# Performance work log

Measured on AMD Instinct MI355X. Metric: run time of the kernel, lower is better.

The kernel has to match this reference:

```python
import jax, jax.numpy as jnp
import numpy as np
from jax import lax

NH = 1024
CATS = 1024
B = 64
T = 512


def setup_inputs() -> dict:
    key = jax.random.key(0)
    ks = jax.random.split(key, 12)
    s_in = 1.0 / np.sqrt(CATS)
    s_h = 1.0 / np.sqrt(NH)
    return {
        "x": jax.random.normal(ks[0], (B, T, CATS), jnp.float32),
        "h0": jax.random.normal(ks[1], (B, NH), jnp.float32),
        # torch Linear weights are [out, in]
        "Wh": jax.random.uniform(ks[2], (NH, CATS), jnp.float32, -s_in, s_in),
        "Wz": jax.random.uniform(ks[3], (NH, CATS), jnp.float32, -s_in, s_in),
        "Wr": jax.random.uniform(ks[4], (NH, CATS), jnp.float32, -s_in, s_in),
        "Uh": jax.random.uniform(ks[5], (NH, NH), jnp.float32, -s_h, s_h),
        "Uz": jax.random.uniform(ks[6], (NH, NH), jnp.float32, -s_h, s_h),
        "Ur": jax.random.uniform(ks[7], (NH, NH), jnp.float32, -s_h, s_h),
        "bz": jax.random.uniform(ks[8], (NH,), jnp.float32, -s_h, s_h),
        "br": jax.random.uniform(ks[9], (NH,), jnp.float32, -s_h, s_h),
        "Wout": jax.random.uniform(ks[10], (CATS, NH), jnp.float32, -s_h, s_h),
    }


def _gru_last_h(x, h0, Wh, Wz, Wr, Uh, Uz, Ur, bz, br):
    # Precompute input projections as big GEMMs: [B,T,nh] each
    xh = jnp.einsum('btc,hc->bth', x, Wh)
    xz = jnp.einsum('btc,hc->bth', x, Wz)
    # Note: reset gate r is computed in the original but NEVER used in htilde
    # (htilde = tanh(Wh x + Uh h)); it does not affect the output, so we omit it.
    # Scan over time: inputs as [T, B, nh]
    seq = (jnp.swapaxes(xh, 0, 1), jnp.swapaxes(xz, 0, 1))

    def step(h, inp):
        xh_t, xz_t = inp
        z = jax.nn.sigmoid(xz_t + h @ Uz.T + bz)
        htilde = jnp.tanh(xh_t + h @ Uh.T)
        h_new = (1.0 - z) * h + z * htilde
        return h_new, None

    hT, _ = lax.scan(step, h0, seq)
    return hT  # [B, nh]


def reference(x, h0, Wh, Wz, Wr, Uh, Uz, Ur, bz, br, Wout):
    hT = _gru_last_h(x, h0, Wh, Wz, Wr, Uh, Uz, Ur, bz, br)
    return hT @ Wout.T  # [B, cats]
```

## Files before the change

kernel.cpp:

```cpp
#include <hip/hip_runtime.h>

typedef __attribute__((ext_vector_type(8))) short short8v;
typedef __attribute__((ext_vector_type(4))) short short4v;
typedef __attribute__((ext_vector_type(4))) float f32x4;
typedef __attribute__((ext_vector_type(4))) float float4v;
typedef unsigned long long u64;

#define NHID 1024
#define NCAT 1024
#define NB   64
#define NT   512

__device__ __forceinline__ short f2bf(float f) {
  union { float f; unsigned u; } c; c.f = f;
  unsigned r = (c.u + 0x7fffu + ((c.u >> 16) & 1u)) >> 16;
  return (short)r;
}

union HF { u64 q[2]; short8v v; };

__device__ __forceinline__ u64 ald(const u64* p) {
  return __hip_atomic_load(p, __ATOMIC_RELAXED, __HIP_MEMORY_SCOPE_AGENT);
}
__device__ __forceinline__ void ast(u64* p, u64 v) {
  __hip_atomic_store(p, v, __ATOMIC_RELAXED, __HIP_MEMORY_SCOPE_AGENT);
}

__global__ void cast_kernel(const float* __restrict__ x, const float* __restrict__ h0,
                            short* __restrict__ xb, short* __restrict__ hb0) {
  const long NX4 = (long)NB * NT * NCAT / 4;
  const long NH4 = (long)NB * NHID / 4;
  long i = (long)blockIdx.x * blockDim.x + threadIdx.x;
  long stride = (long)gridDim.x * blockDim.x;
  for (long j = i; j < NX4 + NH4; j += stride) {
    if (j < NH4) {
      float4v v = ((const float4v*)h0)[j];
      short4v s; s[0]=f2bf(v[0]); s[1]=f2bf(v[1]); s[2]=f2bf(v[2]); s[3]=f2bf(v[3]);
      ((short4v*)hb0)[j] = s;
    } else {
      long jj = j - NH4;
      float4v v = ((const float4v*)x)[jj];
      short4v s; s[0]=f2bf(v[0]); s[1]=f2bf(v[1]); s[2]=f2bf(v[2]); s[3]=f2bf(v[3]);
      ((short4v*)xb)[jj] = s;
    }
  }
}

__global__ __launch_bounds__(256, 1) void gru_kernel(
    const float* __restrict__ h0, const float* __restrict__ Wh, const float* __restrict__ Wz,
    const float* __restrict__ Uh, const float* __restrict__ Uz, const float* __restrict__ bz,
    const float* __restrict__ Wout, const short* __restrict__ xb,
    short* __restrict__ hbuf0, short* __restrict__ hbuf1,
    unsigned* __restrict__ flags, float* __restrict__ out)
{
  extern __shared__ char smem[];
  short8v* ufr = (short8v*)smem;
  float*   red = (float*)(smem + 131072);
  short*   rp  = (short*)(smem + 131072 + 12288);

  const int tid  = threadIdx.x;
  const int lane = tid & 63;
  const int wv   = tid >> 6;
  const int mt   = blockIdx.x >> 6;
  const int cg   = blockIdx.x & 63;
  const int col  = lane & 15;
  const int quad = lane >> 4;
  const int kq   = quad * 8;
  const int jg   = cg * 16 + col;

  for (int idx = tid; idx < 64 * 2 * 64; idx += 256) {
    int l  = idx & 63;
    int nt = (idx >> 6) & 1;
    int kb = idx >> 7;
    int j  = cg * 16 + (l & 15);
    int k0 = (kb & 31) * 32 + (l >> 4) * 8;
    const float* M = (kb < 32) ? (nt ? Uh : Uz) : (nt ? Wh : Wz);
    short8v v;
#pragma unroll
    for (int e = 0; e < 8; ++e) v[e] = f2bf(M[j * 1024 + k0 + e]);
    ufr[idx] = v;
  }
  __syncthreads();

  float hl[4] = {0.f, 0.f, 0.f, 0.f};
  float bzv = 0.f;
  if (wv == 0) {
    bzv = bz[jg];
#pragma unroll
    for (int r = 0; r < 4; ++r) hl[r] = h0[(mt * 16 + quad * 4 + r) * NHID + jg];
  }

  short* hb[2] = { hbuf0, hbuf1 };
  const int kb0 = wv * 16;
  unsigned* myflag = flags + (mt * 64 + cg) * 16;
  const unsigned* pollp  = flags + (mt * 64 + (wv & 1) * 32 + (lane & 31)) * 16;
  const unsigned* pollpt = flags + (mt * 64 + wv * 16 + (lane & 15)) * 16;

  short8v xf[16];
  if (wv >= 2) {
    const short* xrow = xb + ((long)(mt * 16 + col) * NT + 0) * NCAT + (kb0 - 32) * 32 + kq;
#pragma unroll
    for (int i = 0; i < 16; ++i) xf[i] = *(const short8v*)(xrow + i * 32);
  }

  for (int t = 0; t < NT; ++t) {
    const int par = t & 1;
    f32x4 pz = {0.f,0.f,0.f,0.f}, ph = {0.f,0.f,0.f,0.f};

    if (wv < 2) {
      if (t > 0) {
        const unsigned tt = (unsigned)t;
        for (;;) {
          unsigned v = __hip_atomic_load(pollp, __ATOMIC_RELAXED, __HIP_MEMORY_SCOPE_AGENT);
          if (__ballot(v < tt) == 0ull) break;
          __builtin_amdgcn_s_sleep(1);
        }
      }
      const u64* hq = (const u64*)hb[t & 1] + (mt * 16 + col) * 256 + kb0 * 8 + quad * 2;
      u64 q[32];
#pragma unroll
      for (int i = 0; i < 16; ++i) {
        q[2 * i]     = ald(hq + i * 8);
        q[2 * i + 1] = ald(hq + i * 8 + 1);
      }
#pragma unroll
      for (int i = 0; i < 16; ++i) {
        HF f; f.q[0] = q[2 * i]; f.q[1] = q[2 * i + 1];
        int kb = kb0 + i;
        pz = __builtin_amdgcn_mfma_f32_16x16x32_bf16(f.v, ufr[kb * 128 + lane],      pz, 0, 0, 0);
        ph = __builtin_amdgcn_mfma_f32_16x16x32_bf16(f.v, ufr[kb * 128 + 64 + lane], ph, 0, 0, 0);
      }
    } else {
#pragma unroll
      for (int i = 0; i < 16; ++i) {
        int kb = kb0 + i;
        pz = __builtin_amdgcn_mfma_f32_16x16x32_bf16(xf[i], ufr[kb * 128 + lane],      pz, 0, 0, 0);
        ph = __builtin_amdgcn_mfma_f32_16x16x32_bf16(xf[i], ufr[kb * 128 + 64 + lane], ph, 0, 0, 0);
      }
      if (t + 1 < NT) {
        const short* xrow = xb + ((long)(mt * 16 + col) * NT + (t + 1)) * NCAT + (kb0 - 32) * 32 + kq;
#pragma unroll
        for (int i = 0; i < 16; ++i) xf[i] = *(const short8v*)(xrow + i * 32);
      }
    }

    if (wv != 0) {
      float* sl = red + ((par * 3 + (wv - 1)) * 64 + lane) * 8;
      *(f32x4*)sl       = pz;
      *(f32x4*)(sl + 4) = ph;
    }
    __syncthreads();

    if (wv == 0) {
      f32x4 accz = pz, acch = ph;
#pragma unroll
      for (int s = 0; s < 3; ++s) {
        const float* sl = red + ((par * 3 + s) * 64 + lane) * 8;
        accz += *(const f32x4*)sl;
        acch += *(const f32x4*)(sl + 4);
      }
#pragma unroll
      for (int r = 0; r < 4; ++r) {
        float zp = accz[r] + bzv;
        float z  = 1.f / (1.f + __expf(-zp));
        float ht = 2.f / (1.f + __expf(-2.f * acch[r])) - 1.f;
        float v  = hl[r] + z * (ht - hl[r]);
        hl[r] = v;
        rp[(quad * 4 + r) * 16 + col] = f2bf(v);
      }
      __asm__ volatile("s_waitcnt lgkmcnt(0)" ::: "memory");
      u64 val = ((const u64*)rp)[lane];
      u64* hnq = (u64*)hb[(t + 1) & 1];
      ast(hnq + (mt * 16 + (lane >> 2)) * 256 + cg * 4 + (lane & 3), val);
      __asm__ volatile("s_waitcnt vmcnt(0)" ::: "memory");
      if (lane == 0)
        __hip_atomic_store(myflag, (unsigned)(t + 1), __ATOMIC_RELAXED, __HIP_MEMORY_SCOPE_AGENT);
    }
  }

  {
    for (;;) {
      unsigned v = __hip_atomic_load(pollpt, __ATOMIC_RELAXED, __HIP_MEMORY_SCOPE_AGENT);
      if (__ballot(v < (unsigned)NT) == 0ull) break;
      __builtin_amdgcn_s_sleep(1);
    }
    const int kb0t = wv * 8;
    const u64* hq = (const u64*)hbuf0 + (mt * 16 + col) * 256 + kb0t * 8 + quad * 2;
    u64 q[16];
#pragma unroll
    for (int i = 0; i < 8; ++i) {
      q[2 * i]     = ald(hq + i * 8);
      q[2 * i + 1] = ald(hq + i * 8 + 1);
    }
    f32x4 acc = {0.f,0.f,0.f,0.f};
    const float* wrow = Wout + (long)jg * NHID + kb0t * 32 + kq;
#pragma unroll
    for (int kb = 0; kb < 8; ++kb) {
      HF f; f.q[0] = q[2 * kb]; f.q[1] = q[2 * kb + 1];
      float4v w0 = *(const float4v*)(wrow + kb * 32);
      float4v w1 = *(const float4v*)(wrow + kb * 32 + 4);
      short8v b;
      b[0] = f2bf(w0[0]); b[1] = f2bf(w0[1]); b[2] = f2bf(w0[2]); b[3] = f2bf(w0[3]);
      b[4] = f2bf(w1[0]); b[5] = f2bf(w1[1]); b[6] = f2bf(w1[2]); b[7] = f2bf(w1[3]);
      acc = __builtin_amdgcn_mfma_f32_16x16x32_bf16(f.v, b, acc, 0, 0, 0);
    }
    if (wv != 0)
      *(f32x4*)(red + ((wv - 1) * 64 + lane) * 8) = acc;
    __syncthreads();
    if (wv == 0) {
#pragma unroll
      for (int s = 0; s < 3; ++s)
        acc += *(const f32x4*)(red + (s * 64 + lane) * 8);
#pragma unroll
      for (int r = 0; r < 4; ++r)
        out[(mt * 16 + quad * 4 + r) * NCAT + jg] = acc[r];
    }
  }
}

extern "C" void kernel_launch(void* const* d_in, const int* in_sizes, int n_in,
                              void* d_out, int out_size, void* d_ws, size_t ws_size,
                              hipStream_t stream) {
  const float* x    = (const float*)d_in[0];
  const float* h0   = (const float*)d_in[1];
  const float* Wh   = (const float*)d_in[2];
  const float* Wz   = (const float*)d_in[3];
  const float* Uh   = (const float*)d_in[5];
  const float* Uz   = (const float*)d_in[6];
  const float* bz   = (const float*)d_in[8];
  const float* Wout = (const float*)d_in[10];

  char* ws = (char*)d_ws;
  unsigned* flags = (unsigned*)ws;
  short* hb0 = (short*)(ws + 16384);
  short* hb1 = (short*)(ws + 16384 + 131072);
  short* xb  = (short*)(ws + 16384 + 262144);

  hipMemsetAsync(flags, 0, 16384, stream);
  cast_kernel<<<4096, 256, 0, stream>>>(x, h0, xb, hb0);

  hipFuncSetAttribute((const void*)gru_kernel,
                      hipFuncAttributeMaxDynamicSharedMemorySize, 144384);
  gru_kernel<<<256, 256, 144384, stream>>>(h0, Wh, Wz, Uh, Uz, bz, Wout, xb,
                                           hb0, hb1, flags, (float*)d_out);
}
```

Baseline: 2.679 ms.

## Drop cast kernel, convert x in-loop, use per-step hidden-state ring buffer

Removes the separate fp32-to-bf16 cast kernel: the GRU kernel now reads x and h0 as fp32 and converts them in registers. The double-buffered hidden state becomes a ring with one slot per timestep, so slots are never overwritten and the reader can use plain vector loads instead of relaxed atomic 64-bit loads. This removes one full pass over x plus a kernel launch. In exchange the x-prefetch traffic inside the recurrence doubles, and the workspace grows to about 64 MB. Dynamic LDS is also trimmed slightly.

```diff
diff --git a/kernel.cpp b/kernel.cpp
--- a/kernel.cpp
+++ b/kernel.cpp
@@ -1,7 +1,6 @@
 #include <hip/hip_runtime.h>
 
 typedef __attribute__((ext_vector_type(8))) short short8v;
-typedef __attribute__((ext_vector_type(4))) short short4v;
 typedef __attribute__((ext_vector_type(4))) float f32x4;
 typedef __attribute__((ext_vector_type(4))) float float4v;
 typedef unsigned long long u64;
@@ -10,6 +9,7 @@
 #define NCAT 1024
 #define NB   64
 #define NT   512
+#define RING_STRIDE 65536
 
 __device__ __forceinline__ short f2bf(float f) {
   union { float f; unsigned u; } c; c.f = f;
@@ -17,46 +17,29 @@
   return (short)r;
 }
 
-union HF { u64 q[2]; short8v v; };
-
-__device__ __forceinline__ u64 ald(const u64* p) {
-  return __hip_atomic_load(p, __ATOMIC_RELAXED, __HIP_MEMORY_SCOPE_AGENT);
-}
 __device__ __forceinline__ void ast(u64* p, u64 v) {
   __hip_atomic_store(p, v, __ATOMIC_RELAXED, __HIP_MEMORY_SCOPE_AGENT);
 }
 
-__global__ void cast_kernel(const float* __restrict__ x, const float* __restrict__ h0,
-                            short* __restrict__ xb, short* __restrict__ hb0) {
-  const long NX4 = (long)NB * NT * NCAT / 4;
-  const long NH4 = (long)NB * NHID / 4;
-  long i = (long)blockIdx.x * blockDim.x + threadIdx.x;
-  long stride = (long)gridDim.x * blockDim.x;
-  for (long j = i; j < NX4 + NH4; j += stride) {
-    if (j < NH4) {
-      float4v v = ((const float4v*)h0)[j];
-      short4v s; s[0]=f2bf(v[0]); s[1]=f2bf(v[1]); s[2]=f2bf(v[2]); s[3]=f2bf(v[3]);
-      ((short4v*)hb0)[j] = s;
-    } else {
-      long jj = j - NH4;
-      float4v v = ((const float4v*)x)[jj];
-      short4v s; s[0]=f2bf(v[0]); s[1]=f2bf(v[1]); s[2]=f2bf(v[2]); s[3]=f2bf(v[3]);
-      ((short4v*)xb)[jj] = s;
-    }
-  }
+__device__ __forceinline__ short8v cvt8(float4v a, float4v b) {
+  short8v s;
+  s[0]=f2bf(a[0]); s[1]=f2bf(a[1]); s[2]=f2bf(a[2]); s[3]=f2bf(a[3]);
+  s[4]=f2bf(b[0]); s[5]=f2bf(b[1]); s[6]=f2bf(b[2]); s[7]=f2bf(b[3]);
+  return s;
 }
 
 __global__ __launch_bounds__(256, 1) void gru_kernel(
     const float* __restrict__ h0, const float* __restrict__ Wh, const float* __restrict__ Wz,
     const float* __restrict__ Uh, const float* __restrict__ Uz, const float* __restrict__ bz,
-    const float* __restrict__ Wout, const short* __restrict__ xb,
-    short* __restrict__ hbuf0, short* __restrict__ hbuf1,
-    unsigned* __restrict__ flags, float* __restrict__ out)
+    const float* __restrict__ Wout, const float* __restrict__ x,
+    short* __restrict__ ring, unsigned* __restrict__ flags, float* __restrict__ out)
 {
   extern __shared__ char smem[];
   short8v* ufr = (short8v*)smem;
   float*   red = (float*)(smem + 131072);
   short*   rp  = (short*)(smem + 131072 + 12288);
+
+  __builtin_amdgcn_fence(__ATOMIC_ACQUIRE, "agent");
 
   const int tid  = threadIdx.x;
   const int lane = tid & 63;
@@ -90,7 +73,6 @@
     for (int r = 0; r < 4; ++r) hl[r] = h0[(mt * 16 + quad * 4 + r) * NHID + jg];
   }
 
-  short* hb[2] = { hbuf0, hbuf1 };
   const int kb0 = wv * 16;
   unsigned* myflag = flags + (mt * 64 + cg) * 16;
   const unsigned* pollp  = flags + (mt * 64 + (wv & 1) * 32 + (lane & 31)) * 16;
@@ -98,9 +80,10 @@
 
   short8v xf[16];
   if (wv >= 2) {
-    const short* xrow = xb + ((long)(mt * 16 + col) * NT + 0) * NCAT + (kb0 - 32) * 32 + kq;
-#pragma unroll
-    for (int i = 0; i < 16; ++i) xf[i] = *(const short8v*)(xrow + i * 32);
+    const float* xrow = x + ((long)(mt * 16 + col) * NT + 0) * NCAT + (kb0 - 32) * 32 + kq;
+#pragma unroll
+    for (int i = 0; i < 16; ++i)
+      xf[i] = cvt8(*(const float4v*)(xrow + i * 32), *(const float4v*)(xrow + i * 32 + 4));
   }
 
   for (int t = 0; t < NT; ++t) {
@@ -108,6 +91,7 @@
     f32x4 pz = {0.f,0.f,0.f,0.f}, ph = {0.f,0.f,0.f,0.f};
 
     if (wv < 2) {
+      short8v f[16];
       if (t > 0) {
         const unsigned tt = (unsigned)t;
         for (;;) {
@@ -115,20 +99,22 @@
           if (__ballot(v < tt) == 0ull) break;
           __builtin_amdgcn_s_sleep(1);
         }
-      }
-      const u64* hq = (const u64*)hb[t & 1] + (mt * 16 + col) * 256 + kb0 * 8 + quad * 2;
-      u64 q[32];
+        __asm__ volatile("" ::: "memory");
+        const short* hrow = ring + (size_t)t * RING_STRIDE
+                          + (mt * 16 + col) * 1024 + kb0 * 32 + kq;
+#pragma unroll
+        for (int i = 0; i < 16; ++i) f[i] = *(const short8v*)(hrow + i * 32);
+      } else {
+        const float* hrow = h0 + (mt * 16 + col) * NHID + kb0 * 32 + kq;
+#pragma unroll
+        for (int i = 0; i < 16; ++i)
+          f[i] = cvt8(*(const float4v*)(hrow + i * 32), *(const float4v*)(hrow + i * 32 + 4));
+      }
 #pragma unroll
       for (int i = 0; i < 16; ++i) {
-        q[2 * i]     = ald(hq + i * 8);
-        q[2 * i + 1] = ald(hq + i * 8 + 1);
-      }
-#pragma unroll
-      for (int i = 0; i < 16; ++i) {
-        HF f; f.q[0] = q[2 * i]; f.q[1] = q[2 * i + 1];
         int kb = kb0 + i;
-        pz = __builtin_amdgcn_mfma_f32_16x16x32_bf16(f.v, ufr[kb * 128 + lane],      pz, 0, 0, 0);
-        ph = __builtin_amdgcn_mfma_f32_16x16x32_bf16(f.v, ufr[kb * 128 + 64 + lane], ph, 0, 0, 0);
+        pz = __builtin_amdgcn_mfma_f32_16x16x32_bf16(f[i], ufr[kb * 128 + lane],      pz, 0, 0, 0);
+        ph = __builtin_amdgcn_mfma_f32_16x16x32_bf16(f[i], ufr[kb * 128 + 64 + lane], ph, 0, 0, 0);
       }
     } else {
 #pragma unroll
@@ -138,9 +124,10 @@
         ph = __builtin_amdgcn_mfma_f32_16x16x32_bf16(xf[i], ufr[kb * 128 + 64 + lane], ph, 0, 0, 0);
       }
       if (t + 1 < NT) {
-        const short* xrow = xb + ((long)(mt * 16 + col) * NT + (t + 1)) * NCAT + (kb0 - 32) * 32 + kq;
-#pragma unroll
-        for (int i = 0; i < 16; ++i) xf[i] = *(const short8v*)(xrow + i * 32);
+        const float* xrow = x + ((long)(mt * 16 + col) * NT + (t + 1)) * NCAT + (kb0 - 32) * 32 + kq;
+#pragma unroll
+        for (int i = 0; i < 16; ++i)
+          xf[i] = cvt8(*(const float4v*)(xrow + i * 32), *(const float4v*)(xrow + i * 32 + 4));
       }
     }
 
@@ -170,7 +157,7 @@
       }
       __asm__ volatile("s_waitcnt lgkmcnt(0)" ::: "memory");
       u64 val = ((const u64*)rp)[lane];
-      u64* hnq = (u64*)hb[(t + 1) & 1];
+      u64* hnq = (u64*)(ring + (size_t)(t + 1) * RING_STRIDE);
       ast(hnq + (mt * 16 + (lane >> 2)) * 256 + cg * 4 + (lane & 3), val);
       __asm__ volatile("s_waitcnt vmcnt(0)" ::: "memory");
       if (lane == 0)
@@ -184,25 +171,18 @@
       if (__ballot(v < (unsigned)NT) == 0ull) break;
       __builtin_amdgcn_s_sleep(1);
     }
+    __asm__ volatile("" ::: "memory");
     const int kb0t = wv * 8;
-    const u64* hq = (const u64*)hbuf0 + (mt * 16 + col) * 256 + kb0t * 8 + quad * 2;
-    u64 q[16];
-#pragma unroll
-    for (int i = 0; i < 8; ++i) {
-      q[2 * i]     = ald(hq + i * 8);
-      q[2 * i + 1] = ald(hq + i * 8 + 1);
-    }
+    const short* hrow = ring + (size_t)NT * RING_STRIDE
+                      + (mt * 16 + col) * 1024 + kb0t * 32 + kq;
     f32x4 acc = {0.f,0.f,0.f,0.f};
     const float* wrow = Wout + (long)jg * NHID + kb0t * 32 + kq;
 #pragma unroll
     for (int kb = 0; kb < 8; ++kb) {
-      HF f; f.q[0] = q[2 * kb]; f.q[1] = q[2 * kb + 1];
+      short8v a = *(const short8v*)(hrow + kb * 32);
       float4v w0 = *(const float4v*)(wrow + kb * 32);
       float4v w1 = *(const float4v*)(wrow + kb * 32 + 4);
-      short8v b;
-      b[0] = f2bf(w0[0]); b[1] = f2bf(w0[1]); b[2] = f2bf(w0[2]); b[3] = f2bf(w0[3]);
-      b[4] = f2bf(w1[0]); b[5] = f2bf(w1[1]); b[6] = f2bf(w1[2]); b[7] = f2bf(w1[3]);
-      acc = __builtin_amdgcn_mfma_f32_16x16x32_bf16(f.v, b, acc, 0, 0, 0);
+      acc = __builtin_amdgcn_mfma_f32_16x16x32_bf16(a, cvt8(w0, w1), acc, 0, 0, 0);
     }
     if (wv != 0)
       *(f32x4*)(red + ((wv - 1) * 64 + lane) * 8) = acc;
@@ -232,15 +212,12 @@
 
   char* ws = (char*)d_ws;
   unsigned* flags = (unsigned*)ws;
-  short* hb0 = (short*)(ws + 16384);
-  short* hb1 = (short*)(ws + 16384 + 131072);
-  short* xb  = (short*)(ws + 16384 + 262144);
+  short* ring = (short*)(ws + 16384);
 
   hipMemsetAsync(flags, 0, 16384, stream);
-  cast_kernel<<<4096, 256, 0, stream>>>(x, h0, xb, hb0);
 
   hipFuncSetAttribute((const void*)gru_kernel,
-                      hipFuncAttributeMaxDynamicSharedMemorySize, 144384);
-  gru_kernel<<<256, 256, 144384, stream>>>(h0, Wh, Wz, Uh, Uz, bz, Wout, xb,
-                                           hb0, hb1, flags, (float*)d_out);
-}
+                      hipFuncAttributeMaxDynamicSharedMemorySize, 143872);
+  gru_kernel<<<256, 256, 143872, stream>>>(h0, Wh, Wz, Uh, Uz, bz, Wout, x,
+                                           ring, flags, (float*)d_out);
+}
```

Result: faster. 2.384 ms (-11.0%).
